# Kernel optimization log

Hardware: AMD Instinct MI355X
Metric: run time of the kernel (lower is better)

## Reference

```python
import jax, jax.numpy as jnp
import numpy as np
from jax import lax

GROUPS = 4
KH = KW = 3
K = KH * KW
STRIDE = (1, 1)
PAD = ((1, 1), (1, 1))
DIL = (1, 1)


def _bilinear_gather(padded, py, px):
    # padded: (B,C,Hp,Wp); py,px: (B,C,K,Ho,Wo) float sample positions in padded coords
    B, C, Hp, Wp = padded.shape
    bi = jnp.arange(B)[:, None, None, None, None]
    ci = jnp.arange(C)[None, :, None, None, None]
    y0 = jnp.floor(py)
    x0 = jnp.floor(px)
    wy = py - y0
    wx = px - x0
    out = jnp.zeros(py.shape, padded.dtype)
    corners = ((0, 0, (1 - wy) * (1 - wx)), (0, 1, (1 - wy) * wx),
               (1, 0, wy * (1 - wx)), (1, 1, wy * wx))
    for dy, dx, w in corners:
        yy = y0 + dy
        xx = x0 + dx
        valid = (yy >= 0) & (yy < Hp) & (xx >= 0) & (xx < Wp)  # zero outside (implicit zero padding)
        yc = jnp.clip(yy, 0, Hp - 1).astype(jnp.int32)
        xc = jnp.clip(xx, 0, Wp - 1).astype(jnp.int32)
        out = out + jnp.where(valid, padded[bi, ci, yc, xc] * w, 0.0)
    return out


def deform_conv2d(inps, weight, bias, weight_off, bias_off):
    B, C, H, W = inps.shape
    # offset/mask predicting conv (grouped, same geometry as the main conv)
    off = lax.conv_general_dilated(inps, weight_off, STRIDE, PAD, rhs_dilation=DIL,
                                   feature_group_count=GROUPS,
                                   dimension_numbers=('NCHW', 'OIHW', 'NCHW'))
    off = off + bias_off[None, :, None, None]
    Ho, Wo = off.shape[2], off.shape[3]
    off = off.reshape(B, 3, C * K, Ho, Wo)  # (B, dim+1, C*K, Ho, Wo)
    dy = off[:, 0].reshape(B, C, K, Ho, Wo)
    dx = off[:, 1].reshape(B, C, K, Ho, Wo)
    # softmax across the GROUP axis, as in the original reshape(b,1,groups,-1,h,w).softmax(dim=2)
    mask = jax.nn.softmax(off[:, 2].reshape(B, GROUPS, (C // GROUPS) * K, Ho, Wo), axis=1)
    mask = mask.reshape(B, C, K, Ho, Wo)

    padded = jnp.pad(inps, ((0, 0), (0, 0), PAD[0], PAD[1]))
    ky, kx = jnp.meshgrid(jnp.arange(KH), jnp.arange(KW), indexing='ij')
    ky = ky.ravel().astype(inps.dtype)
    kx = kx.ravel().astype(inps.dtype)
    oh = jnp.arange(Ho, dtype=inps.dtype)
    ow = jnp.arange(Wo, dtype=inps.dtype)
    # sample position per (batch, in-channel, kernel tap, output pixel)
    py = oh[None, None, None, :, None] * STRIDE[0] + ky[None, None, :, None, None] * DIL[0] + dy
    px = ow[None, None, None, None, :] * STRIDE[1] + kx[None, None, :, None, None] * DIL[1] + dx

    sampled = _bilinear_gather(padded, py, px) * mask  # (B,C,K,Ho,Wo)

    Cout = weight.shape[0]
    Cg = C // GROUPS
    wg = weight.reshape(GROUPS, Cout // GROUPS, Cg, K)          # (g, o, c, k)
    sg = sampled.reshape(B, GROUPS, Cg, K, Ho, Wo)              # (b, g, c, k, h, w)
    out = jnp.einsum('bgckhw,gock->bgohw', sg, wg).reshape(B, Cout, Ho, Wo)
    return out + bias[None, :, None, None]


def setup_inputs() -> dict:
    key = jax.random.key(0)
    k0, k1, k2, k3 = jax.random.split(key, 4)
    B, C, H, W = 8, 64, 64, 64
    Cout = 64
    inps = jax.random.normal(k0, (B, C, H, W), dtype=jnp.float32)
    weight = jax.random.normal(k1, (Cout, C // GROUPS, KH, KW), dtype=jnp.float32) * 0.05
    bias = jax.random.normal(k2, (Cout,), dtype=jnp.float32) * 0.05
    # small offset-conv weights -> offsets of a few pixels, non-saturated softmax
    weight_off = jax.random.normal(k3, (C * K * 3, C // GROUPS, KH, KW), dtype=jnp.float32) * 0.05
    bias_off = jnp.zeros((C * K * 3,), dtype=jnp.float32)
    return {'inps': inps, 'weight': weight, 'bias': bias,
            'weight_off': weight_off, 'bias_off': bias_off}


def reference(inps, weight, bias, weight_off, bias_off):
    return deform_conv2d(inps, weight, bias, weight_off, bias_off)
```

## Files before the change

kernel.cpp:

```cpp
#include <hip/hip_runtime.h>

typedef __attribute__((ext_vector_type(8))) short short8;
typedef __attribute__((ext_vector_type(4))) float f32x4;

__device__ __forceinline__ unsigned short bf16rne(float f) {
    unsigned u = __float_as_uint(f);
    u += 0x7FFFu + ((u >> 16) & 1u);
    return (unsigned short)(u >> 16);
}
__device__ __forceinline__ float bf16dec(unsigned short h) {
    return __uint_as_float((unsigned)h << 16);
}
__device__ __forceinline__ unsigned cvtpk2(float lo, float hi) {
    unsigned r;
    asm("v_cvt_pk_bf16_f32 %0, %1, %2" : "=v"(r) : "v"(lo), "v"(hi));
    return r;
}
__device__ __forceinline__ unsigned short cvt1(float f) {
    return (unsigned short)cvtpk2(f, f);
}
__device__ __forceinline__ float declo(unsigned u) { return __uint_as_float(u << 16); }
__device__ __forceinline__ float dechi(unsigned u) { return __uint_as_float(u & 0xFFFF0000u); }

extern __shared__ char smem[];


#define IMC10_OFF   0
#define PATCH10_OFF 37376
#define SX10_OFF    55424
#define LGX10_OFF   64128
#define LDS_V10     81536
#define OTB10_OFF   37376

#define LOG2E 1.4426950408889634f

#define PWOFF_U32  138240
#define PWM_U32    5120
#define WS_NEEDED  ((size_t)(PWOFF_U32 + PWM_U32) * 4)

__global__ __launch_bounds__(256)
void pack_weights(const float* __restrict__ wmain,
                  const float* __restrict__ woff,
                  unsigned* __restrict__ pw)
{
    int idx = blockIdx.x * 256 + threadIdx.x;
    if (idx < PWOFF_U32) {
        int j2   = idx & 3;
        int lane = (idx >> 2) & 63;
        int rest = idx >> 8;
        int kt   = rest % 5;
        int t    = rest / 5;
        int comp = t / 36, r36 = t - comp * 36;
        int jw   = r36 / 9, ntg = r36 - jw * 9;
        int ochb = comp * 576 + jw * 144 + ntg * 16;
        int g    = ochb / 432;
        int ktf  = (9 * g) >> 1;
        int och  = ochb + (lane & 15);
        int ck   = (ktf + kt) * 32 + (lane >> 4) * 8 + j2 * 2 - g * 144;
        float v0 = 0.f, v1 = 0.f;
        if ((unsigned)ck < 144u)       v0 = woff[(size_t)och * 144 + ck];
        if ((unsigned)(ck + 1) < 144u) v1 = woff[(size_t)och * 144 + ck + 1];
        pw[idx] = (unsigned)bf16rne(v0) | ((unsigned)bf16rne(v1) << 16);
    } else if (idx < PWOFF_U32 + PWM_U32) {
        int m    = idx - PWOFF_U32;
        int j2   = m & 3;
        int lane = (m >> 2) & 63;
        int rest = m >> 8;
        int jw   = rest / 5, pair = rest - jw * 5;
        int och  = jw * 16 + (lane & 15);
        int w0   = pair * 32 + (lane >> 4) * 8 + j2 * 2;
        float v0 = (w0 < 144)     ? wmain[(size_t)och * 144 + w0]     : 0.f;
        float v1 = (w0 + 1 < 144) ? wmain[(size_t)och * 144 + w0 + 1] : 0.f;
        pw[idx] = (unsigned)bf16rne(v0) | ((unsigned)bf16rne(v1) << 16);
    }
}

__global__ __launch_bounds__(512, 4)
void deform_v10(const float* __restrict__ inps,
                const float* __restrict__ bmain,
                const float* __restrict__ boff,
                const unsigned short* __restrict__ pwoff,
                const unsigned short* __restrict__ pwm,
                float* __restrict__ out)
{
    unsigned short* IMC   = (unsigned short*)(smem + IMC10_OFF);
    unsigned short* PATCH = (unsigned short*)(smem + PATCH10_OFF);
    unsigned short* SX    = (unsigned short*)(smem + SX10_OFF);
    unsigned short* LGX   = (unsigned short*)(smem + LGX10_OFF);
    float*          OTB   = (float*)(smem + OTB10_OFF);

    const int tid  = threadIdx.x;
    const int lane = tid & 63;
    const int wv   = __builtin_amdgcn_readfirstlane(tid >> 6);
    const int jw   = wv & 3;
    const int mtw  = wv >> 2;
    const int slot = lane & 15;
    const int q    = lane >> 4;

    const int b    = blockIdx.x >> 7;
    const int tile = blockIdx.x & 127;
    const int ty0  = (tile >> 3) << 2;
    const int tx0  = (tile & 7) << 3;

    const float* inb = inps + (size_t)b * 262144;

    for (int e = tid; e < 8960; e += 512) {
        int c = e / 140, rem = e - c * 140;
        int y = rem / 14, x = rem - y * 14;
        int gy = ty0 + y - 3, gx = tx0 + x - 3;
        float v = 0.f;
        if ((unsigned)gy < 64u && (unsigned)gx < 64u)
            v = inb[(c * 64 + gy) * 64 + gx];
        PATCH[c * 141 + y * 14 + x] = cvt1(v);
    }
    __syncthreads();

    {
        const int px  = tid >> 4;
        const int sub = tid & 15;
        const int pyr = px >> 3, pxx = px & 7;
        unsigned* dst = (unsigned*)(IMC + px * 584);
        #pragma unroll 3
        for (int i = 0; i < 18; ++i) {
            int u  = i * 16 + sub;
            int kk = u * 2;
            int c0 = kk / 9,        r0 = kk - c0 * 9;
            int c1 = (kk + 1) / 9,  r1 = (kk + 1) - c1 * 9;
            unsigned short a  = PATCH[c0 * 141 + (pyr + r0 / 3 + 2) * 14 + pxx + r0 % 3 + 2];
            unsigned short bb = PATCH[c1 * 141 + (pyr + r1 / 3 + 2) * 14 + pxx + r1 % 3 + 2];
            dst[u] = (unsigned)a | ((unsigned)bb << 16);
        }
    }
    __syncthreads();

    const short8* ap = (const short8*)(smem + IMC10_OFF) + (mtw * 16 + slot) * 73 + q;

    f32x4 aco = {0.f, 0.f, 0.f, 0.f};
    auto pair_mfma = [&](int kt2) {
        const short8 bfr = ((const short8*)pwm)[(jw * 5 + kt2) * 64 + lane];
        const short8 a8  = *(const short8*)(SX + jw * 1088 + (mtw * 16 + slot) * 34 + q * 8);
        aco = __builtin_amdgcn_mfma_f32_16x16x32_bf16(a8, bfr, aco, 0, 0, 0);
    };

    auto gemmpair = [&](int comp, int n0, f32x4& acc0, f32x4& acc1) {
        const int ochb0 = comp * 576 + jw * 144 + n0 * 16;
        const int g     = ochb0 / 432;
        const int ktf   = (9 * g) >> 1;
        const short8* wp0 = (const short8*)pwoff + (comp * 36 + jw * 9 + n0) * 320 + lane;
        const short8* wp1 = wp0 + 320;
        short8 b0[5], b1[5];
        #pragma unroll
        for (int kt = 0; kt < 5; ++kt) { b0[kt] = wp0[kt * 64]; b1[kt] = wp1[kt * 64]; }
        #pragma unroll
        for (int kt = 0; kt < 5; ++kt) {
            const short8 af = ap[(ktf + kt) * 4];
            acc0 = __builtin_amdgcn_mfma_f32_16x16x32_bf16(af, b0[kt], acc0, 0, 0, 0);
            acc1 = __builtin_amdgcn_mfma_f32_16x16x32_bf16(af, b1[kt], acc1, 0, 0, 0);
        }
        const float bo0 = boff[ochb0 + slot];
        const float bo1 = boff[ochb0 + 16 + slot];
        #pragma unroll
        for (int i = 0; i < 4; ++i) { acc0[i] += bo0; acc1[i] += bo1; }
    };

    auto gemmsingle = [&](int comp, int n0, f32x4& acc) {
        const int ochb = comp * 576 + jw * 144 + n0 * 16;
        const int g    = ochb / 432;
        const int ktf  = (9 * g) >> 1;
        const short8* wp = (const short8*)pwoff + (comp * 36 + jw * 9 + n0) * 320 + lane;
        short8 bw[5];
        #pragma unroll
        for (int kt = 0; kt < 5; ++kt) bw[kt] = wp[kt * 64];
        #pragma unroll
        for (int kt = 0; kt < 5; ++kt) {
            const short8 af = ap[(ktf + kt) * 4];
            acc = __builtin_amdgcn_mfma_f32_16x16x32_bf16(af, bw[kt], acc, 0, 0, 0);
        }
        const float bo = boff[ochb + slot];
        #pragma unroll
        for (int i = 0; i < 4; ++i) acc[i] += bo;
    };

    auto expwrite = [&](int ntg, const f32x4& aM, float* er, int lgb) {
        #pragma unroll
        for (int r = 0; r < 4; ++r) {
            er[r] = exp2f(aM[r] * LOG2E);
            int pxr = mtw * 16 + q * 4 + r;
            LGX[lgb + pxr * 136 + (ntg & 1) * 68 + slot * 4 + jw] = cvt1(er[r]);
        }
    };

    auto sample4 = [&](int ntg, const f32x4& aD, const f32x4& aX,
                       const float* er, int lgb) {
        const int rr  = ntg * 16 + slot;
        const int cg  = rr / 9;
        const int kk9 = rr - cg * 9;
        const int kyk = kk9 / 3, kxk = kk9 - kyk * 3;
        const int c   = jw * 16 + cg;
        const float* inc = inb + c * 4096;
        const int pbase = c * 141;
        const int par = ntg & 1;
        const float fyk = (float)(ty0 + kyk - 1);
        const float fxk = (float)(tx0 + kxk - 1);

        #pragma unroll
        for (int r = 0; r < 4; ++r) {
            const int pxr = mtw * 16 + q * 4 + r;
            const int pyr = pxr >> 3, pxx = pxr & 7;

            const uint2 lg = *(const uint2*)(LGX + lgb + pxr * 136 + par * 68 + slot * 4);
            const float s4 = declo(lg.x) + dechi(lg.x) + declo(lg.y) + dechi(lg.y);
            const float msk = er[r] * __builtin_amdgcn_rcpf(s4);

            float pyf = fyk + (float)pyr + aD[r];
            float pxf = fxk + (float)pxx + aX[r];
            float y0f = floorf(pyf), x0f = floorf(pxf);
            float wy = pyf - y0f, wx = pxf - x0f;
            int iy0 = (int)y0f, ix0 = (int)x0f;

            int ly0 = iy0 - ty0 + 3;
            int lx0 = ix0 - tx0 + 3;
            float v;
            if ((unsigned)ly0 < 9u && (unsigned)lx0 < 13u) {
                const int a = pbase + ly0 * 14 + lx0;
                float p00 = bf16dec(PATCH[a]),      p01 = bf16dec(PATCH[a + 1]);
                float p10 = bf16dec(PATCH[a + 14]), p11 = bf16dec(PATCH[a + 15]);
                float top = fmaf(wx, p01 - p00, p00);
                float bot = fmaf(wx, p11 - p10, p10);
                v = fmaf(wy, bot - top, top);
            } else {
                float w00 = (1.f - wy) * (1.f - wx), w01 = (1.f - wy) * wx;
                float w10 = wy * (1.f - wx),         w11 = wy * wx;
                v = 0.f;
                if ((unsigned)iy0 < 64u) {
                    if ((unsigned)ix0 < 64u)       v += w00 * inc[iy0 * 64 + ix0];
                    if ((unsigned)(ix0 + 1) < 64u) v += w01 * inc[iy0 * 64 + ix0 + 1];
                }
                if ((unsigned)(iy0 + 1) < 64u) {
                    if ((unsigned)ix0 < 64u)       v += w10 * inc[(iy0 + 1) * 64 + ix0];
                    if ((unsigned)(ix0 + 1) < 64u) v += w11 * inc[(iy0 + 1) * 64 + ix0 + 1];
                }
            }
            SX[jw * 1088 + pxr * 34 + par * 16 + slot] = cvt1(v * msk);
        }
    };

    for (int p = 0; p < 4; ++p) {
        const int n0  = 2 * p;
        const int lgb = (p & 1) * 4352;

        f32x4 aD0 = {0.f,0.f,0.f,0.f}, aX0 = {0.f,0.f,0.f,0.f}, aM0 = {0.f,0.f,0.f,0.f};
        f32x4 aD1 = {0.f,0.f,0.f,0.f}, aX1 = {0.f,0.f,0.f,0.f}, aM1 = {0.f,0.f,0.f,0.f};
        gemmpair(0, n0, aD0, aD1);
        gemmpair(1, n0, aX0, aX1);
        gemmpair(2, n0, aM0, aM1);

        float er0[4], er1[4];
        expwrite(n0,     aM0, er0, lgb);
        expwrite(n0 + 1, aM1, er1, lgb);
        __syncthreads();

        sample4(n0,     aD0, aX0, er0, lgb);
        sample4(n0 + 1, aD1, aX1, er1, lgb);

        asm volatile("" ::: "memory");
        pair_mfma(p);
    }
    {
        f32x4 aD = {0.f,0.f,0.f,0.f}, aX = {0.f,0.f,0.f,0.f}, aM = {0.f,0.f,0.f,0.f};
        gemmsingle(0, 8, aD);
        gemmsingle(1, 8, aX);
        gemmsingle(2, 8, aM);
        float er[4];
        expwrite(8, aM, er, 0);
        __syncthreads();
        sample4(8, aD, aX, er, 0);
        asm volatile("" ::: "memory");
        pair_mfma(4);
    }
    __syncthreads();

    {
        const int o = jw * 16 + slot;
        const float bo = bmain[o];
        #pragma unroll
        for (int r = 0; r < 4; ++r)
            OTB[o * 33 + mtw * 16 + q * 4 + r] = aco[r] + bo;
    }
    __syncthreads();
    #pragma unroll
    for (int i = 0; i < 4; ++i) {
        int f  = i * 512 + tid;
        int oo = f >> 5, pp = f & 31;
        out[(size_t)(b * 64 + oo) * 4096 + (ty0 + (pp >> 3)) * 64 + (tx0 + (pp & 7))] =
            OTB[oo * 33 + pp];
    }
}

extern "C" void kernel_launch(void* const* d_in, const int* in_sizes, int n_in,
                              void* d_out, int out_size, void* d_ws, size_t ws_size,
                              hipStream_t stream) {
    const float* inps   = (const float*)d_in[0];
    const float* weight = (const float*)d_in[1];
    const float* bias   = (const float*)d_in[2];
    const float* woff   = (const float*)d_in[3];
    const float* boff   = (const float*)d_in[4];
    float* outp = (float*)d_out;

    unsigned* pw = (unsigned*)d_ws;
    pack_weights<<<dim3(560), dim3(256), 0, stream>>>(weight, woff, pw);
    hipFuncSetAttribute((const void*)deform_v10,
                        hipFuncAttributeMaxDynamicSharedMemorySize, LDS_V10);
    deform_v10<<<dim3(1024), dim3(512), LDS_V10, stream>>>(
        inps, bias, boff,
        (const unsigned short*)pw,
        (const unsigned short*)(pw + PWOFF_U32), outp);
    (void)ws_size; (void)in_sizes; (void)n_in; (void)out_size;
}
```

Measured before the change: 125.7 us.

## Restructure offset-conv loop per tap group with prefetched weights and wider patch

Replaces the paired two-tap-group iterations with a single loop over nine tap groups. Each iteration prefetches the next group's offset-conv weight fragments into registers (15 short8) while the current sampling runs. The input patch halo grows from 3 to 4 pixels with a 16-wide row, so more bilinear samples take the shared-memory path instead of the global fallback. LOG2E is folded into the mask weights and bias to drop a multiply before exp2. The cost is a sync per tap group instead of per pair and extra register pressure that could limit occupancy.

```diff
diff --git a/kernel.cpp b/kernel.cpp
--- a/kernel.cpp
+++ b/kernel.cpp
@@ -25,12 +25,12 @@
 extern __shared__ char smem[];
 
 
-#define IMC10_OFF   0
-#define PATCH10_OFF 37376
-#define SX10_OFF    55424
-#define LGX10_OFF   64128
-#define LDS_V10     81536
-#define OTB10_OFF   37376
+#define IMC11_OFF   0
+#define PATCH11_OFF 37376
+#define SX11_OFF    62720
+#define LGX11_OFF   72960
+#define LDS_V11     81664
+#define OTB11_OFF   37376
 
 #define LOG2E 1.4426950408889634f
 
@@ -60,6 +60,7 @@
         float v0 = 0.f, v1 = 0.f;
         if ((unsigned)ck < 144u)       v0 = woff[(size_t)och * 144 + ck];
         if ((unsigned)(ck + 1) < 144u) v1 = woff[(size_t)och * 144 + ck + 1];
+        if (comp == 2) { v0 *= LOG2E; v1 *= LOG2E; }
         pw[idx] = (unsigned)bf16rne(v0) | ((unsigned)bf16rne(v1) << 16);
     } else if (idx < PWOFF_U32 + PWM_U32) {
         int m    = idx - PWOFF_U32;
@@ -76,18 +77,18 @@
 }
 
 __global__ __launch_bounds__(512, 4)
-void deform_v10(const float* __restrict__ inps,
+void deform_v11(const float* __restrict__ inps,
                 const float* __restrict__ bmain,
                 const float* __restrict__ boff,
                 const unsigned short* __restrict__ pwoff,
                 const unsigned short* __restrict__ pwm,
                 float* __restrict__ out)
 {
-    unsigned short* IMC   = (unsigned short*)(smem + IMC10_OFF);
-    unsigned short* PATCH = (unsigned short*)(smem + PATCH10_OFF);
-    unsigned short* SX    = (unsigned short*)(smem + SX10_OFF);
-    unsigned short* LGX   = (unsigned short*)(smem + LGX10_OFF);
-    float*          OTB   = (float*)(smem + OTB10_OFF);
+    unsigned short* IMC   = (unsigned short*)(smem + IMC11_OFF);
+    unsigned short* PATCH = (unsigned short*)(smem + PATCH11_OFF);
+    unsigned short* SX    = (unsigned short*)(smem + SX11_OFF);
+    unsigned short* LGX   = (unsigned short*)(smem + LGX11_OFF);
+    float*          OTB   = (float*)(smem + OTB11_OFF);
 
     const int tid  = threadIdx.x;
     const int lane = tid & 63;
@@ -104,14 +105,14 @@
 
     const float* inb = inps + (size_t)b * 262144;
 
-    for (int e = tid; e < 8960; e += 512) {
-        int c = e / 140, rem = e - c * 140;
-        int y = rem / 14, x = rem - y * 14;
-        int gy = ty0 + y - 3, gx = tx0 + x - 3;
+    for (int e = tid; e < 12288; e += 512) {
+        int c = e / 192, rem = e - c * 192;
+        int y = rem >> 4, x = rem & 15;
+        int gy = ty0 + y - 4, gx = tx0 + x - 4;
         float v = 0.f;
         if ((unsigned)gy < 64u && (unsigned)gx < 64u)
             v = inb[(c * 64 + gy) * 64 + gx];
-        PATCH[c * 141 + y * 14 + x] = cvt1(v);
+        PATCH[c * 198 + rem] = cvt1(v);
     }
     __syncthreads();
 
@@ -126,79 +127,76 @@
             int kk = u * 2;
             int c0 = kk / 9,        r0 = kk - c0 * 9;
             int c1 = (kk + 1) / 9,  r1 = (kk + 1) - c1 * 9;
-            unsigned short a  = PATCH[c0 * 141 + (pyr + r0 / 3 + 2) * 14 + pxx + r0 % 3 + 2];
-            unsigned short bb = PATCH[c1 * 141 + (pyr + r1 / 3 + 2) * 14 + pxx + r1 % 3 + 2];
+            unsigned short a  = PATCH[c0 * 198 + (pyr + r0 / 3 + 3) * 16 + pxx + r0 % 3 + 3];
+            unsigned short bb = PATCH[c1 * 198 + (pyr + r1 / 3 + 3) * 16 + pxx + r1 % 3 + 3];
             dst[u] = (unsigned)a | ((unsigned)bb << 16);
         }
     }
     __syncthreads();
 
-    const short8* ap = (const short8*)(smem + IMC10_OFF) + (mtw * 16 + slot) * 73 + q;
-
     f32x4 aco = {0.f, 0.f, 0.f, 0.f};
-    auto pair_mfma = [&](int kt2) {
-        const short8 bfr = ((const short8*)pwm)[(jw * 5 + kt2) * 64 + lane];
-        const short8 a8  = *(const short8*)(SX + jw * 1088 + (mtw * 16 + slot) * 34 + q * 8);
+
+    auto pair_mfma = [&](int pair) {
+        const short8 bfr = ((const short8*)pwm)[(jw * 5 + pair) * 64 + lane];
+        const short8 a8  = *(const short8*)(SX + jw * 1280 + (mtw * 16 + slot) * 40 + q * 8);
         aco = __builtin_amdgcn_mfma_f32_16x16x32_bf16(a8, bfr, aco, 0, 0, 0);
     };
 
-    auto gemmpair = [&](int comp, int n0, f32x4& acc0, f32x4& acc1) {
-        const int ochb0 = comp * 576 + jw * 144 + n0 * 16;
-        const int g     = ochb0 / 432;
-        const int ktf   = (9 * g) >> 1;
-        const short8* wp0 = (const short8*)pwoff + (comp * 36 + jw * 9 + n0) * 320 + lane;
-        const short8* wp1 = wp0 + 320;
-        short8 b0[5], b1[5];
-        #pragma unroll
-        for (int kt = 0; kt < 5; ++kt) { b0[kt] = wp0[kt * 64]; b1[kt] = wp1[kt * 64]; }
-        #pragma unroll
-        for (int kt = 0; kt < 5; ++kt) {
-            const short8 af = ap[(ktf + kt) * 4];
-            acc0 = __builtin_amdgcn_mfma_f32_16x16x32_bf16(af, b0[kt], acc0, 0, 0, 0);
-            acc1 = __builtin_amdgcn_mfma_f32_16x16x32_bf16(af, b1[kt], acc1, 0, 0, 0);
-        }
-        const float bo0 = boff[ochb0 + slot];
-        const float bo1 = boff[ochb0 + 16 + slot];
-        #pragma unroll
-        for (int i = 0; i < 4; ++i) { acc0[i] += bo0; acc1[i] += bo1; }
+    short8 bwA[15];
+    auto loadB = [&](int ntg) {
+        if (ntg < 9) {
+            #pragma unroll
+            for (int comp = 0; comp < 3; ++comp) {
+                const short8* wp = (const short8*)pwoff +
+                                   (comp * 36 + jw * 9 + ntg) * 320 + lane;
+                #pragma unroll
+                for (int kt = 0; kt < 5; ++kt) bwA[comp * 5 + kt] = wp[kt * 64];
+            }
+        }
     };
-
-    auto gemmsingle = [&](int comp, int n0, f32x4& acc) {
-        const int ochb = comp * 576 + jw * 144 + n0 * 16;
-        const int g    = ochb / 432;
-        const int ktf  = (9 * g) >> 1;
-        const short8* wp = (const short8*)pwoff + (comp * 36 + jw * 9 + n0) * 320 + lane;
-        short8 bw[5];
-        #pragma unroll
-        for (int kt = 0; kt < 5; ++kt) bw[kt] = wp[kt * 64];
-        #pragma unroll
-        for (int kt = 0; kt < 5; ++kt) {
-            const short8 af = ap[(ktf + kt) * 4];
-            acc = __builtin_amdgcn_mfma_f32_16x16x32_bf16(af, bw[kt], acc, 0, 0, 0);
-        }
-        const float bo = boff[ochb + slot];
-        #pragma unroll
-        for (int i = 0; i < 4; ++i) acc[i] += bo;
-    };
-
-    auto expwrite = [&](int ntg, const f32x4& aM, float* er, int lgb) {
+    loadB(0);
+
+    for (int ntg = 0; ntg < 9; ++ntg) {
+        const int lb = (ntg & 1) * 2176;
+
+        f32x4 aD = {0.f,0.f,0.f,0.f};
+        f32x4 aX = {0.f,0.f,0.f,0.f};
+        f32x4 aM = {0.f,0.f,0.f,0.f};
+
+        auto gemm3 = [&](f32x4& acc, int comp) {
+            const int ochb = comp * 576 + jw * 144 + ntg * 16;
+            const int g    = ochb / 432;
+            const int ktf  = (9 * g) >> 1;
+            const short8* ap0 = (const short8*)(smem + IMC11_OFF);
+            #pragma unroll
+            for (int kt = 0; kt < 5; ++kt) {
+                const short8 af = ap0[(mtw * 16 + slot) * 73 + (ktf + kt) * 4 + q];
+                acc = __builtin_amdgcn_mfma_f32_16x16x32_bf16(af, bwA[comp * 5 + kt], acc, 0, 0, 0);
+            }
+            float bo = boff[ochb + slot];
+            if (comp == 2) bo *= LOG2E;
+            acc[0] += bo; acc[1] += bo; acc[2] += bo; acc[3] += bo;
+        };
+        gemm3(aD, 0); gemm3(aX, 1); gemm3(aM, 2);
+
+        loadB(ntg + 1);
+
+        float er[4];
         #pragma unroll
         for (int r = 0; r < 4; ++r) {
-            er[r] = exp2f(aM[r] * LOG2E);
+            er[r] = exp2f(aM[r]);
             int pxr = mtw * 16 + q * 4 + r;
-            LGX[lgb + pxr * 136 + (ntg & 1) * 68 + slot * 4 + jw] = cvt1(er[r]);
-        }
-    };
-
-    auto sample4 = [&](int ntg, const f32x4& aD, const f32x4& aX,
-                       const float* er, int lgb) {
+            LGX[lb + pxr * 68 + slot * 4 + jw] = cvt1(er[r]);
+        }
+        __syncthreads();
+
         const int rr  = ntg * 16 + slot;
         const int cg  = rr / 9;
         const int kk9 = rr - cg * 9;
         const int kyk = kk9 / 3, kxk = kk9 - kyk * 3;
         const int c   = jw * 16 + cg;
         const float* inc = inb + c * 4096;
-        const int pbase = c * 141;
+        const int pbase = c * 198;
         const int par = ntg & 1;
         const float fyk = (float)(ty0 + kyk - 1);
         const float fxk = (float)(tx0 + kxk - 1);
@@ -208,7 +206,7 @@
             const int pxr = mtw * 16 + q * 4 + r;
             const int pyr = pxr >> 3, pxx = pxr & 7;
 
-            const uint2 lg = *(const uint2*)(LGX + lgb + pxr * 136 + par * 68 + slot * 4);
+            const uint2 lg = *(const uint2*)(LGX + lb + pxr * 68 + slot * 4);
             const float s4 = declo(lg.x) + dechi(lg.x) + declo(lg.y) + dechi(lg.y);
             const float msk = er[r] * __builtin_amdgcn_rcpf(s4);
 
@@ -218,13 +216,13 @@
             float wy = pyf - y0f, wx = pxf - x0f;
             int iy0 = (int)y0f, ix0 = (int)x0f;
 
-            int ly0 = iy0 - ty0 + 3;
-            int lx0 = ix0 - tx0 + 3;
+            int ly0 = iy0 - ty0 + 4;
+            int lx0 = ix0 - tx0 + 4;
             float v;
-            if ((unsigned)ly0 < 9u && (unsigned)lx0 < 13u) {
-                const int a = pbase + ly0 * 14 + lx0;
+            if ((unsigned)ly0 < 11u && (unsigned)lx0 < 15u) {
+                const int a = pbase + ly0 * 16 + lx0;
                 float p00 = bf16dec(PATCH[a]),      p01 = bf16dec(PATCH[a + 1]);
-                float p10 = bf16dec(PATCH[a + 14]), p11 = bf16dec(PATCH[a + 15]);
+                float p10 = bf16dec(PATCH[a + 16]), p11 = bf16dec(PATCH[a + 17]);
                 float top = fmaf(wx, p01 - p00, p00);
                 float bot = fmaf(wx, p11 - p10, p10);
                 v = fmaf(wy, bot - top, top);
@@ -241,42 +239,11 @@
                     if ((unsigned)(ix0 + 1) < 64u) v += w11 * inc[(iy0 + 1) * 64 + ix0 + 1];
                 }
             }
-            SX[jw * 1088 + pxr * 34 + par * 16 + slot] = cvt1(v * msk);
-        }
-    };
-
-    for (int p = 0; p < 4; ++p) {
-        const int n0  = 2 * p;
-        const int lgb = (p & 1) * 4352;
-
-        f32x4 aD0 = {0.f,0.f,0.f,0.f}, aX0 = {0.f,0.f,0.f,0.f}, aM0 = {0.f,0.f,0.f,0.f};
-        f32x4 aD1 = {0.f,0.f,0.f,0.f}, aX1 = {0.f,0.f,0.f,0.f}, aM1 = {0.f,0.f,0.f,0.f};
-        gemmpair(0, n0, aD0, aD1);
-        gemmpair(1, n0, aX0, aX1);
-        gemmpair(2, n0, aM0, aM1);
-
-        float er0[4], er1[4];
-        expwrite(n0,     aM0, er0, lgb);
-        expwrite(n0 + 1, aM1, er1, lgb);
-        __syncthreads();
-
-        sample4(n0,     aD0, aX0, er0, lgb);
-        sample4(n0 + 1, aD1, aX1, er1, lgb);
-
-        asm volatile("" ::: "memory");
-        pair_mfma(p);
-    }
-    {
-        f32x4 aD = {0.f,0.f,0.f,0.f}, aX = {0.f,0.f,0.f,0.f}, aM = {0.f,0.f,0.f,0.f};
-        gemmsingle(0, 8, aD);
-        gemmsingle(1, 8, aX);
-        gemmsingle(2, 8, aM);
-        float er[4];
-        expwrite(8, aM, er, 0);
-        __syncthreads();
-        sample4(8, aD, aX, er, 0);
-        asm volatile("" ::: "memory");
-        pair_mfma(4);
+            SX[jw * 1280 + pxr * 40 + par * 16 + slot] = cvt1(v * msk);
+        }
+
+        if (ntg & 1)  { asm volatile("" ::: "memory"); pair_mfma(ntg >> 1); }
+        if (ntg == 8) { asm volatile("" ::: "memory"); pair_mfma(4); }
     }
     __syncthreads();
 
@@ -309,9 +276,9 @@
 
     unsigned* pw = (unsigned*)d_ws;
     pack_weights<<<dim3(560), dim3(256), 0, stream>>>(weight, woff, pw);
-    hipFuncSetAttribute((const void*)deform_v10,
-                        hipFuncAttributeMaxDynamicSharedMemorySize, LDS_V10);
-    deform_v10<<<dim3(1024), dim3(512), LDS_V10, stream>>>(
+    hipFuncSetAttribute((const void*)deform_v11,
+                        hipFuncAttributeMaxDynamicSharedMemorySize, LDS_V11);
+    deform_v11<<<dim3(1024), dim3(512), LDS_V11, stream>>>(
         inps, bias, boff,
         (const unsigned short*)pw,
         (const unsigned short*)(pw + PWOFF_U32), outp);
```

Measured after the change: 130.0 us. 3.4% more time.
